# Kernel tuning notes

Measured on AMD Instinct MI355X. Metric: run time of the kernel, lower is better.

The kernel has to match this reference:

```python
import jax, jax.numpy as jnp
import numpy as np
import math

H = 1024        # number of SSM copies (d_model)
N_HALF = 32     # stored state size (N//2 due to conjugate symmetry)
CHANNELS = 1
SEQ_L = 4096
DT_MIN, DT_MAX = 1e-3, 1e-1


def setup_inputs() -> dict:
    key = jax.random.key(0)
    k1, k2, k3, k4, k5 = jax.random.split(key, 5)
    # log_dt ~ Uniform[log(dt_min), log(dt_max)] as in SSKernel.__init__
    log_dt = jax.random.uniform(k1, (H,), dtype=jnp.float32) \
        * (math.log(DT_MAX) - math.log(DT_MIN)) + math.log(DT_MIN)
    # complex params stored as real (..., 2) views (torch.view_as_real)
    B_ri = jax.random.normal(k2, (H, N_HALF, 2), dtype=jnp.float32)
    C_ri = jax.random.normal(k3, (CHANNELS, H, N_HALF, 2), dtype=jnp.float32)
    # inv_A_real = log(-clamp(A_real, max=-1e-4)); sample A_real ~ -0.5 (S4D-Lin)
    inv_A_real = jnp.log(0.5 * jnp.ones((H, N_HALF), dtype=jnp.float32))
    inv_A_real = inv_A_real + 0.01 * jax.random.normal(k4, (H, N_HALF), dtype=jnp.float32)
    # A_imag = pi * n (S4D-Lin init)
    A_imag = jnp.tile(math.pi * jnp.arange(N_HALF, dtype=jnp.float32), (H, 1))
    A_imag = A_imag + 0.01 * jax.random.normal(k5, (H, N_HALF), dtype=jnp.float32)
    return {"log_dt": log_dt, "B_ri": B_ri, "C_ri": C_ri,
            "inv_A_real": inv_A_real, "A_imag": A_imag, "L": SEQ_L}


def _r2c(x):
    return jax.lax.complex(x[..., 0], x[..., 1])


def reference(log_dt, B_ri, C_ri, inv_A_real, A_imag, L):
    """SSKernelDiag.forward (S4D, bilinear discretization, state=None, rate=1)."""
    dt = jnp.exp(log_dt)                       # (H,)
    C = _r2c(C_ri)                             # (C, H, N) complex
    B = _r2c(B_ri)                             # (H, N) complex
    A = -jnp.exp(inv_A_real) + 1j * A_imag     # (H, N) complex
    dtA = A * dt[:, None]                      # (H, N)
    # C <- (B * C) / (1 - dtA/2) * dt
    C_eff = (B[None] * C) * (1.0 / (1.0 - dtA / 2)) * dt[:, None]  # (C, H, N)
    dA = (1.0 + dtA / 2) / (1.0 - dtA / 2)     # (H, N) bilinear transform
    log_dA = jnp.log(dA)
    # log-Vandermonde: K[c,h,l] = 2 * Re( sum_n C_eff[c,h,n] * dA[h,n]^l )
    ell = jnp.arange(L, dtype=jnp.float32)
    V = jnp.exp(log_dA[:, :, None] * ell)      # (H, N, L) complex
    K = 2.0 * jnp.einsum('chn,hnl->chl', C_eff, V).real  # (C, H, L) float32
    return K
```

## Files before the change

kernel.cpp:

```cpp
#include <hip/hip_runtime.h>


#define HDIM    1024
#define NSTATE  32
#define SEQ_L   4096
#define TPB     256
#define JCOUNT  (SEQ_L / TPB)

__global__ __launch_bounds__(TPB) void sskernel_diag(
    const float* __restrict__ log_dt,
    const float* __restrict__ B_ri,
    const float* __restrict__ C_ri,
    const float* __restrict__ inv_A_real,
    const float* __restrict__ A_imag,
    float* __restrict__ out)
{
    __shared__ float2 s_lo[NSTATE][16];
    __shared__ float2 s_hi[NSTATE][16];
    __shared__ float2 s_step[NSTATE];
    __shared__ float2 s_ceff[NSTATE];

    const int h   = blockIdx.x;
    const int tid = threadIdx.x;

    if (tid < NSTATE) {
        const int n   = tid;
        const int idx = h * NSTATE + n;

        const float dt   = expf(log_dt[h]);
        const float Ar   = -expf(inv_A_real[idx]);
        const float Ai   = A_imag[idx];
        const float dtAr = Ar * dt;
        const float dtAi = Ai * dt;

        const float dr = 1.0f - 0.5f * dtAr;
        const float di =       -0.5f * dtAi;
        const float nr = 1.0f + 0.5f * dtAr;
        const float ni =        0.5f * dtAi;
        const float inv_den = 1.0f / (dr * dr + di * di);

        const float dAr = (nr * dr + ni * di) * inv_den;
        const float dAi = (ni * dr - nr * di) * inv_den;

        const float br = B_ri[2 * idx], bi = B_ri[2 * idx + 1];
        const float cr = C_ri[2 * idx], ci = C_ri[2 * idx + 1];
        const float bcr = br * cr - bi * ci;
        const float bci = br * ci + bi * cr;
        const float scale = 2.0f * dt * inv_den;
        s_ceff[n] = make_float2((bcr * dr + bci * di) * scale,
                                (bci * dr - bcr * di) * scale);

        float pr = 1.0f, pi = 0.0f;
        #pragma unroll
        for (int t = 0; t < 16; ++t) {
            s_lo[n][t] = make_float2(pr, pi);
            const float tr = pr * dAr - pi * dAi;
            pi = pr * dAi + pi * dAr;
            pr = tr;
        }
        const float g16r = pr, g16i = pi;

        float qr = 1.0f, qi = 0.0f;
        #pragma unroll
        for (int t = 0; t < 16; ++t) {
            s_hi[n][t] = make_float2(qr, qi);
            const float tr = qr * g16r - qi * g16i;
            qi = qr * g16i + qi * g16r;
            qr = tr;
        }
        s_step[n] = make_float2(qr, qi);
    }
    __syncthreads();

    float acc[JCOUNT];
    #pragma unroll
    for (int j = 0; j < JCOUNT; ++j) acc[j] = 0.0f;

    const int i_lo = tid & 15;
    const int i_hi = tid >> 4;

    #pragma unroll 4
    for (int n = 0; n < NSTATE; ++n) {
        const float2 lo = s_lo[n][i_lo];
        const float2 hi = s_hi[n][i_hi];
        const float2 st = s_step[n];
        const float2 ce = s_ceff[n];

        float pr = lo.x * hi.x - lo.y * hi.y;
        float pi = lo.x * hi.y + lo.y * hi.x;

        #pragma unroll
        for (int j = 0; j < JCOUNT; ++j) {
            acc[j] += ce.x * pr - ce.y * pi;
            const float tr = pr * st.x - pi * st.y;
            pi = pr * st.y + pi * st.x;
            pr = tr;
        }
    }

    float* o = out + (size_t)h * SEQ_L + tid;
    #pragma unroll
    for (int j = 0; j < JCOUNT; ++j) o[j * TPB] = acc[j];
}

extern "C" void kernel_launch(void* const* d_in, const int* in_sizes, int n_in,
                              void* d_out, int out_size, void* d_ws, size_t ws_size,
                              hipStream_t stream) {
    const float* log_dt     = (const float*)d_in[0];
    const float* B_ri       = (const float*)d_in[1];
    const float* C_ri       = (const float*)d_in[2];
    const float* inv_A_real = (const float*)d_in[3];
    const float* A_imag     = (const float*)d_in[4];
    float* out = (float*)d_out;

    sskernel_diag<<<HDIM, TPB, 0, stream>>>(log_dt, B_ri, C_ri,
                                            inv_A_real, A_imag, out);
}
```

Before: 95.55 us.

## Replace complex power recurrence with real second-order recurrence and split L across blocks

The inner loop no longer advances a complex power and projects it onto C each step. It runs a real two-term linear recurrence, c_{j+2} = 2Re(s)·c_{j+1} − |s|²·c_j, seeded from two precomputed complex coefficients. This cuts the per-step FLOPs roughly in half. Each head is also split into two blocks covering half of L, which doubles the grid and halves the accumulator registers per thread. The cost is duplicated setup work per block, and the three-term real recurrence may accumulate rounding error differently from the complex multiply.

```diff
diff --git a/kernel.cpp b/kernel.cpp
--- a/kernel.cpp
+++ b/kernel.cpp
@@ -5,7 +5,9 @@
 #define NSTATE  32
 #define SEQ_L   4096
 #define TPB     256
-#define JCOUNT  (SEQ_L / TPB)
+#define LSPLIT  2
+#define LCHUNK  (SEQ_L / LSPLIT)
+#define JCOUNT  (LCHUNK / TPB)
 
 __global__ __launch_bounds__(TPB) void sskernel_diag(
     const float* __restrict__ log_dt,
@@ -17,11 +19,13 @@
 {
     __shared__ float2 s_lo[NSTATE][16];
     __shared__ float2 s_hi[NSTATE][16];
-    __shared__ float2 s_step[NSTATE];
-    __shared__ float2 s_ceff[NSTATE];
+    __shared__ float2 s_rec[NSTATE];
+    __shared__ float2 s_ceA[NSTATE];
+    __shared__ float2 s_ceB[NSTATE];
 
-    const int h   = blockIdx.x;
-    const int tid = threadIdx.x;
+    const int h    = blockIdx.x >> 1;
+    const int half = blockIdx.x & 1;
+    const int tid  = threadIdx.x;
 
     if (tid < NSTATE) {
         const int n   = tid;
@@ -47,8 +51,8 @@
         const float bcr = br * cr - bi * ci;
         const float bci = br * ci + bi * cr;
         const float scale = 2.0f * dt * inv_den;
-        s_ceff[n] = make_float2((bcr * dr + bci * di) * scale,
-                                (bci * dr - bcr * di) * scale);
+        float cer = (bcr * dr + bci * di) * scale;
+        float cei = (bci * dr - bcr * di) * scale;
 
         float pr = 1.0f, pi = 0.0f;
         #pragma unroll
@@ -68,7 +72,22 @@
             qi = qr * g16i + qi * g16r;
             qr = tr;
         }
-        s_step[n] = make_float2(qr, qi);
+        s_rec[n] = make_float2(2.0f * qr, -(qr * qr + qi * qi));
+
+        if (half) {
+            float rr = qr, ri = qi;
+            #pragma unroll
+            for (int t = 0; t < 3; ++t) {
+                const float tr = rr * rr - ri * ri;
+                ri = 2.0f * rr * ri;
+                rr = tr;
+            }
+            const float tr = cer * rr - cei * ri;
+            cei = cer * ri + cei * rr;
+            cer = tr;
+        }
+        s_ceA[n] = make_float2(cer, cei);
+        s_ceB[n] = make_float2(cer * qr - cei * qi, cer * qi + cei * qr);
     }
     __syncthreads();
 
@@ -81,24 +100,30 @@
 
     #pragma unroll 4
     for (int n = 0; n < NSTATE; ++n) {
-        const float2 lo = s_lo[n][i_lo];
-        const float2 hi = s_hi[n][i_hi];
-        const float2 st = s_step[n];
-        const float2 ce = s_ceff[n];
+        const float2 lo  = s_lo[n][i_lo];
+        const float2 hi  = s_hi[n][i_hi];
+        const float2 ceA = s_ceA[n];
+        const float2 ceB = s_ceB[n];
+        const float2 rec = s_rec[n];
 
-        float pr = lo.x * hi.x - lo.y * hi.y;
-        float pi = lo.x * hi.y + lo.y * hi.x;
+        const float pr = lo.x * hi.x - lo.y * hi.y;
+        const float pi = lo.x * hi.y + lo.y * hi.x;
+
+        float c0 = ceA.x * pr - ceA.y * pi;
+        float c1 = ceB.x * pr - ceB.y * pi;
+        acc[0] += c0;
+        acc[1] += c1;
 
         #pragma unroll
-        for (int j = 0; j < JCOUNT; ++j) {
-            acc[j] += ce.x * pr - ce.y * pi;
-            const float tr = pr * st.x - pi * st.y;
-            pi = pr * st.y + pi * st.x;
-            pr = tr;
+        for (int j = 2; j < JCOUNT; ++j) {
+            const float c2 = rec.x * c1 + rec.y * c0;
+            acc[j] += c2;
+            c0 = c1;
+            c1 = c2;
         }
     }
 
-    float* o = out + (size_t)h * SEQ_L + tid;
+    float* o = out + (size_t)h * SEQ_L + half * LCHUNK + tid;
     #pragma unroll
     for (int j = 0; j < JCOUNT; ++j) o[j * TPB] = acc[j];
 }
@@ -113,6 +138,6 @@
     const float* A_imag     = (const float*)d_in[4];
     float* out = (float*)d_out;
 
-    sskernel_diag<<<HDIM, TPB, 0, stream>>>(log_dt, B_ri, C_ri,
-                                            inv_A_real, A_imag, out);
+    sskernel_diag<<<HDIM * LSPLIT, TPB, 0, stream>>>(log_dt, B_ri, C_ri,
+                                                     inv_A_real, A_imag, out);
 }
```

Result: faster. 86.21 us (-9.8%).

## Replace complex power recurrence with real second-order linear recurrence

Applied to the files above, without the earlier changes.

Instead of advancing a complex power and taking the real part of C_eff times it, the inner loop now uses the fact that Re(c*z^k) satisfies a real two-term recurrence x_{k+2} = 2Re(w) x_{k+1} - |w|^2 x_k with w = dA^256. C_eff is folded into the low table, and the first two terms are precomputed from packed float4 tables. This cuts the per-step inner work from about six FLOPs to two FMAs. In exchange, setup work is split across 64 threads, and long real recurrences may accumulate rounding differently from the complex form.

```diff
diff --git a/kernel.cpp b/kernel.cpp
--- a/kernel.cpp
+++ b/kernel.cpp
@@ -15,17 +15,16 @@
     const float* __restrict__ A_imag,
     float* __restrict__ out)
 {
-    __shared__ float2 s_lo[NSTATE][16];
-    __shared__ float2 s_hi[NSTATE][16];
-    __shared__ float2 s_step[NSTATE];
-    __shared__ float2 s_ceff[NSTATE];
+    __shared__ float4 s_loR[NSTATE][16];
+    __shared__ float4 s_hh[NSTATE][16];
 
     const int h   = blockIdx.x;
     const int tid = threadIdx.x;
 
-    if (tid < NSTATE) {
-        const int n   = tid;
-        const int idx = h * NSTATE + n;
+    if (tid < 2 * NSTATE) {
+        const int n    = tid & (NSTATE - 1);
+        const int role = tid >> 5;
+        const int idx  = h * NSTATE + n;
 
         const float dt   = expf(log_dt[h]);
         const float Ar   = -expf(inv_A_real[idx]);
@@ -35,40 +34,65 @@
 
         const float dr = 1.0f - 0.5f * dtAr;
         const float di =       -0.5f * dtAi;
+        const float inv_den = 1.0f / (dr * dr + di * di);
+
         const float nr = 1.0f + 0.5f * dtAr;
         const float ni =        0.5f * dtAi;
-        const float inv_den = 1.0f / (dr * dr + di * di);
-
         const float dAr = (nr * dr + ni * di) * inv_den;
         const float dAi = (ni * dr - nr * di) * inv_den;
 
-        const float br = B_ri[2 * idx], bi = B_ri[2 * idx + 1];
-        const float cr = C_ri[2 * idx], ci = C_ri[2 * idx + 1];
-        const float bcr = br * cr - bi * ci;
-        const float bci = br * ci + bi * cr;
-        const float scale = 2.0f * dt * inv_den;
-        s_ceff[n] = make_float2((bcr * dr + bci * di) * scale,
-                                (bci * dr - bcr * di) * scale);
+        if (role == 0) {
+            float sr = dAr, si = dAi;
+            #pragma unroll
+            for (int t = 0; t < 8; ++t) {
+                const float tr = sr * sr - si * si;
+                si = 2.0f * sr * si;
+                sr = tr;
+            }
+            const float recx = 2.0f * sr;
+            const float recy = -(sr * sr + si * si);
 
-        float pr = 1.0f, pi = 0.0f;
-        #pragma unroll
-        for (int t = 0; t < 16; ++t) {
-            s_lo[n][t] = make_float2(pr, pi);
-            const float tr = pr * dAr - pi * dAi;
-            pi = pr * dAi + pi * dAr;
-            pr = tr;
+            const float br = B_ri[2 * idx], bi = B_ri[2 * idx + 1];
+            const float cr = C_ri[2 * idx], ci = C_ri[2 * idx + 1];
+            const float bcr = br * cr - bi * ci;
+            const float bci = br * ci + bi * cr;
+            const float scale = 2.0f * dt * inv_den;
+            float pr = (bcr * dr + bci * di) * scale;
+            float pi = (bci * dr - bcr * di) * scale;
+
+            #pragma unroll
+            for (int t = 0; t < 16; ++t) {
+                s_loR[n][t] = make_float4(pr, pi, recx, recy);
+                const float tr = pr * dAr - pi * dAi;
+                pi = pr * dAi + pi * dAr;
+                pr = tr;
+            }
+        } else {
+            float er = dAr, ei = dAi;
+            #pragma unroll
+            for (int t = 0; t < 4; ++t) {
+                const float tr = er * er - ei * ei;
+                ei = 2.0f * er * ei;
+                er = tr;
+            }
+            float sr = er, si = ei;
+            #pragma unroll
+            for (int t = 0; t < 4; ++t) {
+                const float tr = sr * sr - si * si;
+                si = 2.0f * sr * si;
+                sr = tr;
+            }
+            float qr = 1.0f, qi = 0.0f;
+            #pragma unroll
+            for (int u = 0; u < 16; ++u) {
+                s_hh[n][u] = make_float4(qr, qi,
+                                         qr * sr - qi * si,
+                                         qr * si + qi * sr);
+                const float tr = qr * er - qi * ei;
+                qi = qr * ei + qi * er;
+                qr = tr;
+            }
         }
-        const float g16r = pr, g16i = pi;
-
-        float qr = 1.0f, qi = 0.0f;
-        #pragma unroll
-        for (int t = 0; t < 16; ++t) {
-            s_hi[n][t] = make_float2(qr, qi);
-            const float tr = qr * g16r - qi * g16i;
-            qi = qr * g16i + qi * g16r;
-            qr = tr;
-        }
-        s_step[n] = make_float2(qr, qi);
     }
     __syncthreads();
 
@@ -81,20 +105,20 @@
 
     #pragma unroll 4
     for (int n = 0; n < NSTATE; ++n) {
-        const float2 lo = s_lo[n][i_lo];
-        const float2 hi = s_hi[n][i_hi];
-        const float2 st = s_step[n];
-        const float2 ce = s_ceff[n];
+        const float4 LR = s_loR[n][i_lo];
+        const float4 HH = s_hh[n][i_hi];
 
-        float pr = lo.x * hi.x - lo.y * hi.y;
-        float pi = lo.x * hi.y + lo.y * hi.x;
+        float c0 = LR.x * HH.x - LR.y * HH.y;
+        float c1 = LR.x * HH.z - LR.y * HH.w;
+        acc[0] += c0;
+        acc[1] += c1;
 
         #pragma unroll
-        for (int j = 0; j < JCOUNT; ++j) {
-            acc[j] += ce.x * pr - ce.y * pi;
-            const float tr = pr * st.x - pi * st.y;
-            pi = pr * st.y + pi * st.x;
-            pr = tr;
+        for (int j = 2; j < JCOUNT; ++j) {
+            const float c2 = LR.z * c1 + LR.w * c0;
+            acc[j] += c2;
+            c0 = c1;
+            c1 = c2;
         }
     }
 
```

Result: faster. 84.72 us (-11.3%).
